# Performance work log

Hardware: AMD Instinct MI355X
Metric: run time of the kernel (lower is better)

The kernel has to match this reference:

```python
import jax, jax.numpy as jnp
import numpy as np
from jax import lax

T_STEPS = 40
BATCH = 2048
UNITS = 1024
INPUT_DIM = 1024
Q_BASIS = 8
ORDER = 4  # skfda BSpline default (cubic)


def bspline_basis(ts, q, k=ORDER):
    """Cox-de Boor B-spline basis, n_basis=q, order k, domain [0,1]. ts: (T,) -> (T,q)."""
    ts = np.asarray(ts, dtype=np.float64)
    breaks = np.linspace(0.0, 1.0, q - k + 2)
    knots = np.concatenate([np.zeros(k - 1), breaks, np.ones(k - 1)])  # len q+k
    n0 = len(knots) - 1
    N = np.zeros((len(ts), n0))
    for i in range(n0):
        N[:, i] = ((ts >= knots[i]) & (ts < knots[i + 1])).astype(np.float64)
    for d in range(1, k):
        Nn = np.zeros((len(ts), n0 - d))
        for i in range(n0 - d):
            out = np.zeros(len(ts))
            den1 = knots[i + d] - knots[i]
            if den1 > 0:
                out += (ts - knots[i]) / den1 * N[:, i]
            den2 = knots[i + d + 1] - knots[i + 1]
            if den2 > 0:
                out += (knots[i + d + 1] - ts) / den2 * N[:, i + 1]
            Nn[:, i] = out
        N = Nn
    # at right endpoint t==1 only the last basis is nonzero (value 1)
    at_end = ts >= 1.0 - 1e-12
    N[at_end] = 0.0
    N[at_end, -1] = 1.0
    return N.astype(np.float32)


def setup_inputs() -> dict:
    key = jax.random.key(0)
    k1, k2, k3 = jax.random.split(key, 3)
    D = UNITS + INPUT_DIM
    x = jax.random.normal(k1, (BATCH, T_STEPS, INPUT_DIM), dtype=jnp.float32)
    h0 = jnp.zeros((BATCH, UNITS), dtype=jnp.float32)
    Qw = jax.random.normal(k2, (D, Q_BASIS * UNITS), dtype=jnp.float32) / np.sqrt(D)
    bias = jax.random.uniform(k3, (UNITS,), dtype=jnp.float32, minval=-0.05, maxval=0.05)
    Bt_all = jnp.asarray(bspline_basis(np.linspace(0.0, 1.0, T_STEPS), Q_BASIS))
    return {"x": x, "h0": h0, "Qw": Qw, "bias": bias, "Bt_all": Bt_all}


def reference(x, h0, Qw, bias, Bt_all):
    B, T, I = x.shape
    U = h0.shape[-1]
    q = Bt_all.shape[-1]
    D = Qw.shape[0]
    # block_diag(Bt,...,Bt).T contraction == reshape Q to (D, U, q) and contract q with Bt
    Qr = Qw.reshape(D, U, q)
    W_all = jnp.einsum('duq,tq->tdu', Qr, Bt_all)  # (T, D, U) per-step weight matrices

    def step(h, xw):
        x_t, W_t = xw                       # (B,I), (D,U)
        cat = jnp.concatenate([h, x_t], axis=-1)  # (B, U+I) = (B, D); state first, as in cell
        h_new = jnp.tanh(cat @ W_t + bias)
        return h_new, h_new

    xs = jnp.swapaxes(x, 0, 1)              # (T, B, I)
    _, hs = lax.scan(step, h0, (xs, W_all))
    return jnp.swapaxes(hs, 0, 1)           # (B, T, U)
```

## Files before the change

kernel.cpp:

```cpp
#include <hip/hip_runtime.h>
#include <hip/hip_fp16.h>

#define TS 40
#define NB 2048
#define NU 1024
#define NI 1024
#define ND 2048
#define UD (1024 * 2048)

typedef _Float16 half8 __attribute__((ext_vector_type(8)));
typedef _Float16 half4v __attribute__((ext_vector_type(4)));
typedef float floatx4 __attribute__((ext_vector_type(4)));

__device__ __forceinline__ float tanh_fast(float v) {
  float e = __expf(2.0f * v);
  return 1.0f - 2.0f / (e + 1.0f);
}

__device__ __forceinline__ void gload16(const void* g, void* l) {
  __builtin_amdgcn_global_load_lds(
      (const __attribute__((address_space(1))) void*)g,
      (__attribute__((address_space(3))) void*)l, 16, 0, 0);
}

__device__ __forceinline__ int tile_off(int r, int c8) {
  return (((((r >> 4) * 2 + (c8 >> 2)) << 6) + ((c8 & 3) << 4) + (r & 15)) << 4);
}


__global__ __launch_bounds__(256) void prep_all(
    const float* __restrict__ Qw, const float* __restrict__ Bt,
    _Float16* __restrict__ W,
    const float* __restrict__ x, _Float16* __restrict__ X,
    const float* __restrict__ h0, _Float16* __restrict__ hb)
{
  __shared__ char shm[66816];
  const int tid = threadIdx.x;
  const int bid = blockIdx.x;

  if (bid < 512) {
    _Float16* ldsQ = (_Float16*)shm;
    float* ldsB = (float*)(shm + 65536);
    const int kt = bid & 31;
    const int ut = bid >> 5;
    for (int i = tid; i < TS * 8; i += 256) ldsB[i] = Bt[i];
    const float* qb = Qw + (size_t)(kt * 64) * 8192 + ut * 512;
#pragma unroll
    for (int i = 0; i < 32; ++i) {
      int s = i * 256 + tid;
      int dk = s >> 7, c4 = s & 127;
      float4 v = *(const float4*)(qb + (size_t)dk * 8192 + c4 * 4);
      _Float16* d = &ldsQ[dk * 512 + c4 * 4];
      d[0] = (_Float16)v.x; d[1] = (_Float16)v.y;
      d[2] = (_Float16)v.z; d[3] = (_Float16)v.w;
    }
    __syncthreads();
    const int w = tid >> 6, lane = tid & 63;
    const int dur = lane & 7, ko = lane >> 3;
#pragma unroll 1
    for (int sp = 0; sp < 2; ++sp) {
      const int stripe = w * 2 + sp;
      const int du = stripe * 8 + dur;
      float Q[8][8];
#pragma unroll
      for (int j = 0; j < 8; ++j)
#pragma unroll
        for (int q = 0; q < 8; ++q)
          Q[j][q] = (float)ldsQ[(ko * 8 + j) * 512 + du * 8 + q];
      const int obase = tile_off(du, ko);
#pragma unroll 1
      for (int t = 0; t < TS; ++t) {
        float b[8];
#pragma unroll
        for (int q = 0; q < 8; ++q) b[q] = ldsB[t * 8 + q];
        half8 v;
#pragma unroll
        for (int j = 0; j < 8; ++j) {
          float s = 0.f;
#pragma unroll
          for (int q = 0; q < 8; ++q) s += Q[j][q] * b[q];
          v[j] = (_Float16)s;
        }
        size_t tile = ((size_t)t * 16 + ut) * 32 + kt;
        *(half8*)((char*)W + tile * 8192 + obase) = v;
      }
    }
  } else if (bid < 1792) {
    char* stage = shm;
    const int b2 = bid - 512;
    const int bt = b2 & 31, t = b2 >> 5;
    char* outb = (char*)X + ((size_t)(t * 32 + bt) * 16) * 8192;
    const int r = tid >> 2, cq = tid & 3;
#pragma unroll 1
    for (int kt = 0; kt < 16; ++kt) {
      const float* src =
          x + (size_t)(bt * 64 + r) * (TS * NI) + (size_t)t * NI + kt * 64 + cq * 16;
      float4 a0 = *(const float4*)(src);
      float4 a1 = *(const float4*)(src + 4);
      float4 a2 = *(const float4*)(src + 8);
      float4 a3 = *(const float4*)(src + 12);
      half8 h0v, h1v;
      h0v[0] = (_Float16)a0.x; h0v[1] = (_Float16)a0.y;
      h0v[2] = (_Float16)a0.z; h0v[3] = (_Float16)a0.w;
      h0v[4] = (_Float16)a1.x; h0v[5] = (_Float16)a1.y;
      h0v[6] = (_Float16)a1.z; h0v[7] = (_Float16)a1.w;
      h1v[0] = (_Float16)a2.x; h1v[1] = (_Float16)a2.y;
      h1v[2] = (_Float16)a2.z; h1v[3] = (_Float16)a2.w;
      h1v[4] = (_Float16)a3.x; h1v[5] = (_Float16)a3.y;
      h1v[6] = (_Float16)a3.z; h1v[7] = (_Float16)a3.w;
      *(half8*)(stage + tile_off(r, cq * 2)) = h0v;
      *(half8*)(stage + tile_off(r, cq * 2 + 1)) = h1v;
      __syncthreads();
      uint4 v0 = *(const uint4*)(stage + tid * 32);
      uint4 v1 = *(const uint4*)(stage + tid * 32 + 16);
      *(uint4*)(outb + (size_t)kt * 8192 + tid * 32) = v0;
      *(uint4*)(outb + (size_t)kt * 8192 + tid * 32 + 16) = v1;
      __syncthreads();
    }
  } else {
    int g = (bid - 1792) * 256 + tid;
    int tile_id = g >> 9, rc = g & 511;
    int bt = tile_id >> 4, kt = tile_id & 15;
    int r = rc >> 3, c8 = rc & 7;
    const float* src = h0 + (size_t)(bt * 64 + r) * NU + kt * 64 + c8 * 8;
    float4 v0 = *(const float4*)src;
    float4 v1 = *(const float4*)(src + 4);
    half8 h;
    h[0] = (_Float16)v0.x; h[1] = (_Float16)v0.y;
    h[2] = (_Float16)v0.z; h[3] = (_Float16)v0.w;
    h[4] = (_Float16)v1.x; h[5] = (_Float16)v1.y;
    h[6] = (_Float16)v1.z; h[7] = (_Float16)v1.w;
    *(half8*)((char*)hb + (size_t)tile_id * 8192 + tile_off(r, c8)) = h;
  }
}

__global__ __launch_bounds__(256) void xproj4(
    const _Float16* __restrict__ X, const _Float16* __restrict__ W,
    const float* __restrict__ bias, _Float16* __restrict__ pre)
{
  __shared__ char lds[65536];
  const int tid = threadIdx.x;
  const int bt2 = blockIdx.x;
  const int ut2 = blockIdx.y;
  const int t   = blockIdx.z;
  const int lane = tid & 63, w = tid >> 6;
  const int wm2 = w >> 1, wn2 = w & 1;
  const int l15 = lane & 15, lk = lane >> 4;

  const char* Xb = (const char*)X + (((size_t)t * 32 + bt2 * 2) * 16) * 8192;
  const char* Wb = (const char*)W + (((size_t)t * 16 + ut2 * 2) * 32 + 16) * 8192;

  float bv[4];
#pragma unroll
  for (int nf = 0; nf < 4; ++nf)
    bv[nf] = bias[ut2 * 128 + wn2 * 64 + nf * 16 + l15];

  auto issue = [&](int p) {
    const char* src = (w < 2)
        ? Xb + (size_t)w * (16 * 8192) + (size_t)p * 8192
        : Wb + (size_t)(w - 2) * (32 * 8192) + (size_t)p * 8192;
    src += lane * 16;
    char* dst = lds + (p & 1) * 32768 + w * 8192;
#pragma unroll
    for (int i = 0; i < 8; ++i) gload16(src + i * 1024, dst + i * 1024);
  };

  floatx4 acc[4][4] = {};

  auto comp = [&](int p) {
    const char* pA = lds + (p & 1) * 32768 + wm2 * 8192;
    const char* pB = lds + (p & 1) * 32768 + 16384 + wn2 * 8192;
    __builtin_amdgcn_s_setprio(1);
#pragma unroll
    for (int kk = 0; kk < 2; ++kk) {
      half8 af[4], bf[4];
#pragma unroll
      for (int mf = 0; mf < 4; ++mf)
        af[mf] = *(const half8*)(pA + ((mf * 2 + kk) << 10) + lane * 16);
#pragma unroll
      for (int nf = 0; nf < 4; ++nf)
        bf[nf] = *(const half8*)(pB + ((nf * 2 + kk) << 10) + lane * 16);
#pragma unroll
      for (int mf = 0; mf < 4; ++mf)
#pragma unroll
        for (int nf = 0; nf < 4; ++nf)
          acc[mf][nf] = __builtin_amdgcn_mfma_f32_16x16x32_f16(
              af[mf], bf[nf], acc[mf][nf], 0, 0, 0);
    }
    __builtin_amdgcn_s_setprio(0);
  };

  issue(0);
#pragma unroll 1
  for (int p = 0; p < 16; ++p) {
    if (p + 1 < 16) {
      issue(p + 1);
      asm volatile("s_waitcnt vmcnt(8)" ::: "memory");
    } else {
      asm volatile("s_waitcnt vmcnt(0)" ::: "memory");
    }
    __builtin_amdgcn_s_barrier();
    comp(p);
    __builtin_amdgcn_s_barrier();
  }

  char* pbase = (char*)pre + (size_t)t * (512 * 8192);
#pragma unroll
  for (int ws_ = 0; ws_ < 4; ++ws_) {
    int wmS = ws_ >> 1, wnS = ws_ & 1;
    _Float16 hv[16];
#pragma unroll
    for (int mfl = 0; mfl < 2; ++mfl)
#pragma unroll
      for (int nfl = 0; nfl < 2; ++nfl) {
        int mfp = wmS * 2 + mfl, nfp = wnS * 2 + nfl;
#pragma unroll
        for (int j = 0; j < 4; ++j)
          hv[((mfl * 2 + nfl) << 2) + j] = (_Float16)(acc[mfp][nfp][j] + bv[nfp]);
      }
    int bidS = (bt2 * 2 + wm2) + 32 * (ut2 * 2 + wn2);
    int tidS = ws_ * 64 + lane;
    char* dst = pbase + ((size_t)bidS * 256 + tidS) * 32;
    *(uint4*)dst = ((const uint4*)hv)[0];
    *(uint4*)(dst + 16) = ((const uint4*)hv)[1];
  }
}

__global__ __launch_bounds__(256) void serial5(
    const _Float16* __restrict__ Wh,
    const _Float16* __restrict__ pret,
    const _Float16* __restrict__ hprev,
    _Float16* __restrict__ hnext,
    float* __restrict__ outt)
{
  __shared__ uint4 lds4[4096];
  const int tid = threadIdx.x, bid = blockIdx.x;
  const int bt = bid & 31, ut = bid >> 5;
  const int bidS = bt + 32 * ut;
  const int lane = tid & 63, w = tid >> 6;
  const int wm = w >> 1, wn = w & 1;
  const int l15 = lane & 15, lk = lane >> 4;
  const int b0 = bt * 64, u0 = ut * 64;

  uint4 prv0, prv1;
  {
    const uint4* pp = (const uint4*)((const char*)pret +
                                     ((size_t)bidS * 256 + tid) * 32);
    prv0 = pp[0];
    prv1 = pp[1];
  }

  const char* Hb = (const char*)hprev + (size_t)bt * 16 * 8192;
  const char* Wb = (const char*)Wh + (size_t)ut * 32 * 8192;

  auto issue = [&](int kt) {
    char* la = (char*)lds4 + (kt & 3) * 16384 + w * 2048;
    const char* ga = Hb + (size_t)kt * 8192 + w * 2048 + lane * 16;
    const char* gb = Wb + (size_t)kt * 8192 + w * 2048 + lane * 16;
    gload16(ga, la);
    gload16(ga + 1024, la + 1024);
    gload16(gb, la + 8192);
    gload16(gb + 1024, la + 8192 + 1024);
  };

  floatx4 acc[2][2] = {};

  issue(0);
  issue(1);
  issue(2);
#pragma unroll 1
  for (int p = 0; p < 16; ++p) {
    if (p < 14)       asm volatile("s_waitcnt vmcnt(8)" ::: "memory");
    else if (p == 14) asm volatile("s_waitcnt vmcnt(4)" ::: "memory");
    else              asm volatile("s_waitcnt vmcnt(0)" ::: "memory");
    __builtin_amdgcn_s_barrier();
    if (p + 3 < 16) issue(p + 3);
    const char* pA = (const char*)lds4 + (p & 3) * 16384;
    const char* pB = pA + 8192;
    __builtin_amdgcn_s_setprio(1);
#pragma unroll
    for (int kk = 0; kk < 2; ++kk) {
      half8 af[2], bf[2];
#pragma unroll
      for (int mf = 0; mf < 2; ++mf)
        af[mf] = *(const half8*)(pA + ((((wm * 2 + mf) * 2 + kk) << 10) + lane * 16));
#pragma unroll
      for (int nf = 0; nf < 2; ++nf)
        bf[nf] = *(const half8*)(pB + ((((wn * 2 + nf) * 2 + kk) << 10) + lane * 16));
#pragma unroll
      for (int mf = 0; mf < 2; ++mf)
#pragma unroll
        for (int nf = 0; nf < 2; ++nf)
          acc[mf][nf] = __builtin_amdgcn_mfma_f32_16x16x32_f16(
              af[mf], bf[nf], acc[mf][nf], 0, 0, 0);
    }
    __builtin_amdgcn_s_setprio(0);
  }

  _Float16 prh[16];
  *(uint4*)&prh[0] = prv0;
  *(uint4*)&prh[8] = prv1;
#pragma unroll
  for (int mf = 0; mf < 2; ++mf)
#pragma unroll
    for (int nf = 0; nf < 2; ++nf) {
      int u = u0 + wn * 32 + nf * 16 + l15;
      int brow = b0 + wm * 32 + mf * 16 + (lk << 2);
#pragma unroll
      for (int j = 0; j < 4; ++j) {
        int b = brow + j;
        float p = (float)prh[((mf * 2 + nf) << 2) + j];
        float v = tanh_fast(acc[mf][nf][j] + p);
        outt[(size_t)b * (TS * NU) + u] = v;
        *(_Float16*)((char*)hnext + (((size_t)(bt * 16 + ut)) << 13) +
                     tile_off(b & 63, (u & 63) >> 3) + (u & 7) * 2) = (_Float16)v;
      }
    }
}

__global__ __launch_bounds__(256) void wprep_lin(
    const float* __restrict__ Qw, const float* __restrict__ Bt,
    _Float16* __restrict__ W, int t0, int nt)
{
  __shared__ float ldsQ[32 * 257];
  __shared__ float ldsB[TS * 8];
  const int tid = threadIdx.x;
  const int k0 = blockIdx.x * 32;
  const int u0 = blockIdx.y * 32;
  for (int i = tid; i < TS * 8; i += 256) ldsB[i] = Bt[i];
  const float* qbase = Qw + (size_t)k0 * 8192 + (size_t)u0 * 8;
#pragma unroll
  for (int i = 0; i < 8; ++i) {
    int s = i * 256 + tid;
    int r = s >> 6, c4 = s & 63;
    float4 v = *(const float4*)(qbase + (size_t)r * 8192 + c4 * 4);
    float* d = &ldsQ[r * 257 + c4 * 4];
    d[0] = v.x; d[1] = v.y; d[2] = v.z; d[3] = v.w;
  }
  __syncthreads();
  const int kl = tid & 31;
  const int ug = tid >> 5;
#pragma unroll
  for (int p = 0; p < 4; ++p) {
    int uu = p * 8 + ug;
    float q[8];
#pragma unroll
    for (int j = 0; j < 8; ++j) q[j] = ldsQ[kl * 257 + uu * 8 + j];
    size_t obase = (size_t)(u0 + uu) * 2048 + k0 + kl;
    for (int tt = 0; tt < nt; ++tt) {
      const float* bt = &ldsB[(t0 + tt) * 8];
      float v = 0.f;
#pragma unroll
      for (int j = 0; j < 8; ++j) v += q[j] * bt[j];
      W[(size_t)tt * UD + obase] = (_Float16)v;
    }
  }
}

__global__ __launch_bounds__(256) void step_gemm(
    const float* __restrict__ xt, const float* __restrict__ hp, long hstride,
    const _Float16* __restrict__ Wt, const float* __restrict__ bias,
    float* __restrict__ outt)
{
  __shared__ _Float16 ldsA[2][64 * 64];
  __shared__ _Float16 ldsB[2][128 * 64];
  const int tid = threadIdx.x;
  const int b0 = blockIdx.x * 64;
  const int u0 = blockIdx.y * 128;
  const int lane = tid & 63;
  const int wv = tid >> 6;
  const int wm = wv >> 1, wn = wv & 1;
  const int l15 = lane & 15, lk = lane >> 4;

  float4 areg[4];
  uint4 breg[4];

  auto stage_load = [&](int kt) {
    const int k0 = kt * 64;
    const float* src; size_t stride; int koff;
    if (k0 < NU) { src = hp; stride = (size_t)hstride; koff = k0; }
    else { src = xt; stride = (size_t)TS * NI; koff = k0 - NU; }
#pragma unroll
    for (int i = 0; i < 4; ++i) {
      int s = i * 256 + tid;
      int r = s >> 4, c4 = s & 15;
      areg[i] = *(const float4*)(src + (size_t)(b0 + r) * stride + koff + c4 * 4);
    }
    const _Float16* wsrc = Wt + (size_t)u0 * 2048 + k0;
#pragma unroll
    for (int i = 0; i < 4; ++i) {
      int s = i * 256 + tid;
      int u = s >> 3, c8 = s & 7;
      breg[i] = *(const uint4*)(wsrc + (size_t)u * 2048 + c8 * 8);
    }
  };

  auto stage_write = [&](int buf) {
    char* pA = (char*)&ldsA[buf][0];
    char* pB = (char*)&ldsB[buf][0];
#pragma unroll
    for (int i = 0; i < 4; ++i) {
      int s = i * 256 + tid;
      int r = s >> 4, c4 = s & 15;
      half4v h;
      h[0] = (_Float16)areg[i].x; h[1] = (_Float16)areg[i].y;
      h[2] = (_Float16)areg[i].z; h[3] = (_Float16)areg[i].w;
      int off = (r * 128 + c4 * 8) ^ ((r & 7) << 4);
      *(half4v*)(pA + off) = h;
    }
#pragma unroll
    for (int i = 0; i < 4; ++i) {
      int s = i * 256 + tid;
      int u = s >> 3, c8 = s & 7;
      int off = (u * 128 + c8 * 16) ^ ((u & 7) << 4);
      *(uint4*)(pB + off) = breg[i];
    }
  };

  floatx4 acc[2][4] = {};

  auto compute = [&](int buf) {
    const char* pA = (const char*)&ldsA[buf][0];
    const char* pB = (const char*)&ldsB[buf][0];
#pragma unroll
    for (int kk = 0; kk < 2; ++kk) {
      half8 af[2], bf[4];
#pragma unroll
      for (int mf = 0; mf < 2; ++mf) {
        int r = wm * 32 + mf * 16 + l15;
        int off = r * 128 + ((((kk << 2) | lk) ^ (r & 7)) << 4);
        af[mf] = *(const half8*)(pA + off);
      }
#pragma unroll
      for (int nf = 0; nf < 4; ++nf) {
        int u = wn * 64 + nf * 16 + l15;
        int off = u * 128 + ((((kk << 2) | lk) ^ (u & 7)) << 4);
        bf[nf] = *(const half8*)(pB + off);
      }
#pragma unroll
      for (int mf = 0; mf < 2; ++mf)
#pragma unroll
        for (int nf = 0; nf < 4; ++nf)
          acc[mf][nf] =
              __builtin_amdgcn_mfma_f32_16x16x32_f16(af[mf], bf[nf], acc[mf][nf], 0, 0, 0);
    }
  };

  stage_load(0);
  stage_write(0);
  __syncthreads();
#pragma unroll 1
  for (int kt = 0; kt < 32; ++kt) {
    int cur = kt & 1;
    if (kt + 1 < 32) stage_load(kt + 1);
    compute(cur);
    if (kt + 1 < 32) stage_write(cur ^ 1);
    __syncthreads();
  }

#pragma unroll
  for (int mf = 0; mf < 2; ++mf)
#pragma unroll
    for (int nf = 0; nf < 4; ++nf) {
      int u = u0 + wn * 64 + nf * 16 + l15;
      float bv = bias[u];
      int brow = b0 + wm * 32 + mf * 16 + (lk << 2);
#pragma unroll
      for (int j = 0; j < 4; ++j) {
        float prev = acc[mf][nf][j] + bv;
        outt[(size_t)(brow + j) * (TS * NU) + u] = tanh_fast(prev);
      }
    }
}

extern "C" void kernel_launch(void* const* d_in, const int* in_sizes, int n_in,
                              void* d_out, int out_size, void* d_ws, size_t ws_size,
                              hipStream_t stream) {
  const float* x    = (const float*)d_in[0];
  const float* h0   = (const float*)d_in[1];
  const float* Qw   = (const float*)d_in[2];
  const float* bias = (const float*)d_in[3];
  const float* Bt   = (const float*)d_in[4];
  float* out = (float*)d_out;

  char* ws = (char*)d_ws;
  const size_t w_bytes    = (size_t)UD * TS * sizeof(_Float16);
  const size_t x_bytes    = w_bytes;
  const size_t pre_bytes  = w_bytes;
  const size_t slot_bytes = (size_t)NB * NU * sizeof(_Float16);
  const size_t need = w_bytes + x_bytes + pre_bytes + 2 * slot_bytes;

  if (ws_size >= need) {
    _Float16* W   = (_Float16*)ws;
    _Float16* X   = (_Float16*)(ws + w_bytes);
    _Float16* pre = (_Float16*)(ws + w_bytes + x_bytes);
    _Float16* hb  = (_Float16*)(ws + w_bytes + x_bytes + pre_bytes);
    const size_t SLOT = (size_t)NB * NU;

    prep_all<<<dim3(2816), 256, 0, stream>>>(Qw, Bt, W, x, X, h0, hb);
    xproj4<<<dim3(16, 8, TS), 256, 0, stream>>>(X, W, bias, pre);

    for (int t = 0; t < TS; ++t) {
      const _Float16* hprev = hb + (size_t)(t & 1) * SLOT;
      _Float16* hnext = hb + (size_t)((t + 1) & 1) * SLOT;
      serial5<<<dim3(512), 256, 0, stream>>>(
          W + (size_t)t * UD, pre + (size_t)t * SLOT, hprev, hnext,
          out + (size_t)t * NU);
    }
  } else {
    _Float16* W = (_Float16*)ws;
    const bool big = ws_size >= w_bytes;
    if (big) wprep_lin<<<dim3(64, 32), 256, 0, stream>>>(Qw, Bt, W, 0, TS);
    for (int t = 0; t < TS; ++t) {
      const _Float16* Wtp;
      if (big) {
        Wtp = W + (size_t)t * UD;
      } else {
        wprep_lin<<<dim3(64, 32), 256, 0, stream>>>(Qw, Bt, W, t, 1);
        Wtp = W;
      }
      const float* hp = (t == 0) ? h0 : out + (size_t)(t - 1) * NU;
      long hstride = (t == 0) ? NU : (long)TS * NU;
      step_gemm<<<dim3(32, 8), 256, 0, stream>>>(
          x + (size_t)t * NI, hp, hstride, Wtp, bias, out + (size_t)t * NU);
    }
  }
}
```

Measured before the change: 940.2 us.

## Split serial recurrent step across 8 waves per block instead of 4

```diff
diff --git a/kernel.cpp b/kernel.cpp
--- a/kernel.cpp
+++ b/kernel.cpp
@@ -205,28 +205,24 @@
   }
 
   char* pbase = (char*)pre + (size_t)t * (512 * 8192);
-#pragma unroll
-  for (int ws_ = 0; ws_ < 4; ++ws_) {
-    int wmS = ws_ >> 1, wnS = ws_ & 1;
-    _Float16 hv[16];
-#pragma unroll
-    for (int mfl = 0; mfl < 2; ++mfl)
-#pragma unroll
-      for (int nfl = 0; nfl < 2; ++nfl) {
-        int mfp = wmS * 2 + mfl, nfp = wnS * 2 + nfl;
-#pragma unroll
-        for (int j = 0; j < 4; ++j)
-          hv[((mfl * 2 + nfl) << 2) + j] = (_Float16)(acc[mfp][nfp][j] + bv[nfp]);
-      }
-    int bidS = (bt2 * 2 + wm2) + 32 * (ut2 * 2 + wn2);
-    int tidS = ws_ * 64 + lane;
-    char* dst = pbase + ((size_t)bidS * 256 + tidS) * 32;
-    *(uint4*)dst = ((const uint4*)hv)[0];
-    *(uint4*)(dst + 16) = ((const uint4*)hv)[1];
-  }
-}
-
-__global__ __launch_bounds__(256) void serial5(
+  const int bidS = (bt2 * 2 + wm2) + 32 * (ut2 * 2 + wn2);
+#pragma unroll
+  for (int k = 0; k < 2; ++k)
+#pragma unroll
+    for (int nfp = 0; nfp < 4; ++nfp) {
+      _Float16 hv[8];
+#pragma unroll
+      for (int j = 0; j < 4; ++j) {
+        hv[j]     = (_Float16)(acc[2 * k][nfp][j] + bv[nfp]);
+        hv[4 + j] = (_Float16)(acc[2 * k + 1][nfp][j] + bv[nfp]);
+      }
+      int wS = k * 4 + nfp;
+      char* dst = pbase + ((size_t)bidS * 512 + wS * 64 + lane) * 16;
+      *(uint4*)dst = ((const uint4*)hv)[0];
+    }
+}
+
+__global__ __launch_bounds__(512) void serial6(
     const _Float16* __restrict__ Wh,
     const _Float16* __restrict__ pret,
     const _Float16* __restrict__ hprev,
@@ -238,16 +234,15 @@
   const int bt = bid & 31, ut = bid >> 5;
   const int bidS = bt + 32 * ut;
   const int lane = tid & 63, w = tid >> 6;
-  const int wm = w >> 1, wn = w & 1;
+  const int wm = w >> 2, wn = w & 3;
   const int l15 = lane & 15, lk = lane >> 4;
   const int b0 = bt * 64, u0 = ut * 64;
 
-  uint4 prv0, prv1;
+  uint4 prv;
   {
     const uint4* pp = (const uint4*)((const char*)pret +
-                                     ((size_t)bidS * 256 + tid) * 32);
-    prv0 = pp[0];
-    prv1 = pp[1];
+                                     ((size_t)bidS * 512 + tid) * 16);
+    prv = pp[0];
   }
 
   const char* Hb = (const char*)hprev + (size_t)bt * 16 * 8192;
@@ -255,23 +250,22 @@
 
   auto issue = [&](int kt) {
     char* la = (char*)lds4 + (kt & 3) * 16384 + w * 2048;
-    const char* ga = Hb + (size_t)kt * 8192 + w * 2048 + lane * 16;
-    const char* gb = Wb + (size_t)kt * 8192 + w * 2048 + lane * 16;
-    gload16(ga, la);
-    gload16(ga + 1024, la + 1024);
-    gload16(gb, la + 8192);
-    gload16(gb + 1024, la + 8192 + 1024);
+    const char* g = (w < 4)
+        ? Hb + (size_t)kt * 8192 + w * 2048 + lane * 16
+        : Wb + (size_t)kt * 8192 + (w - 4) * 2048 + lane * 16;
+    gload16(g, la);
+    gload16(g + 1024, la + 1024);
   };
 
-  floatx4 acc[2][2] = {};
+  floatx4 acc[2] = {};
 
   issue(0);
   issue(1);
   issue(2);
 #pragma unroll 1
   for (int p = 0; p < 16; ++p) {
-    if (p < 14)       asm volatile("s_waitcnt vmcnt(8)" ::: "memory");
-    else if (p == 14) asm volatile("s_waitcnt vmcnt(4)" ::: "memory");
+    if (p < 14)       asm volatile("s_waitcnt vmcnt(4)" ::: "memory");
+    else if (p == 14) asm volatile("s_waitcnt vmcnt(2)" ::: "memory");
     else              asm volatile("s_waitcnt vmcnt(0)" ::: "memory");
     __builtin_amdgcn_s_barrier();
     if (p + 3 < 16) issue(p + 3);
@@ -280,42 +274,36 @@
     __builtin_amdgcn_s_setprio(1);
 #pragma unroll
     for (int kk = 0; kk < 2; ++kk) {
-      half8 af[2], bf[2];
+      half8 af[2], bf;
 #pragma unroll
       for (int mf = 0; mf < 2; ++mf)
         af[mf] = *(const half8*)(pA + ((((wm * 2 + mf) * 2 + kk) << 10) + lane * 16));
-#pragma unroll
-      for (int nf = 0; nf < 2; ++nf)
-        bf[nf] = *(const half8*)(pB + ((((wn * 2 + nf) * 2 + kk) << 10) + lane * 16));
+      bf = *(const half8*)(pB + (((wn * 2 + kk) << 10) + lane * 16));
 #pragma unroll
       for (int mf = 0; mf < 2; ++mf)
-#pragma unroll
-        for (int nf = 0; nf < 2; ++nf)
-          acc[mf][nf] = __builtin_amdgcn_mfma_f32_16x16x32_f16(
-              af[mf], bf[nf], acc[mf][nf], 0, 0, 0);
+        acc[mf] = __builtin_amdgcn_mfma_f32_16x16x32_f16(af[mf], bf, acc[mf], 0, 0, 0);
     }
     __builtin_amdgcn_s_setprio(0);
   }
 
-  _Float16 prh[16];
-  *(uint4*)&prh[0] = prv0;
-  *(uint4*)&prh[8] = prv1;
-#pragma unroll
-  for (int mf = 0; mf < 2; ++mf)
-#pragma unroll
-    for (int nf = 0; nf < 2; ++nf) {
-      int u = u0 + wn * 32 + nf * 16 + l15;
+  _Float16 prh[8];
+  *(uint4*)&prh[0] = prv;
+  {
+    int u = u0 + wn * 16 + l15;
+#pragma unroll
+    for (int mf = 0; mf < 2; ++mf) {
       int brow = b0 + wm * 32 + mf * 16 + (lk << 2);
 #pragma unroll
       for (int j = 0; j < 4; ++j) {
         int b = brow + j;
-        float p = (float)prh[((mf * 2 + nf) << 2) + j];
-        float v = tanh_fast(acc[mf][nf][j] + p);
+        float p = (float)prh[mf * 4 + j];
+        float v = tanh_fast(acc[mf][j] + p);
         outt[(size_t)b * (TS * NU) + u] = v;
         *(_Float16*)((char*)hnext + (((size_t)(bt * 16 + ut)) << 13) +
                      tile_off(b & 63, (u & 63) >> 3) + (u & 7) * 2) = (_Float16)v;
       }
     }
+  }
 }
 
 __global__ __launch_bounds__(256) void wprep_lin(
@@ -503,7 +491,7 @@
     for (int t = 0; t < TS; ++t) {
       const _Float16* hprev = hb + (size_t)(t & 1) * SLOT;
       _Float16* hnext = hb + (size_t)((t + 1) & 1) * SLOT;
-      serial5<<<dim3(512), 256, 0, stream>>>(
+      serial6<<<dim3(512), 512, 0, stream>>>(
           W + (size_t)t * UD, pre + (size_t)t * SLOT, hprev, hnext,
           out + (size_t)t * NU);
     }
```

After: 922.2 us, median of 2. About the same (-1.9%).
